# Kernel tuning notes

Hardware: AMD Instinct MI355X
Metric: run time of the kernel (lower is better)

## Reference

```python
import jax, jax.numpy as jnp
import numpy as np

NU, NI, D, E = 100000, 50000, 128, 800000

FLOAT_NAMES = ["emb_user", "emb_item"]
for _l in (1, 2):
    FLOAT_NAMES += [f"l{_l}_ui_pW1", f"l{_l}_ui_pb1", f"l{_l}_ui_pW2", f"l{_l}_ui_pb2"]
    for _e in ("ui", "iu"):
        FLOAT_NAMES += [f"l{_l}_{_e}_Wn", f"l{_l}_{_e}_bn", f"l{_l}_{_e}_Ws", f"l{_l}_{_e}_bs"]
FLOAT_NAMES += ["head_W", "head_b"]


def setup_inputs() -> dict:
    key = jax.random.key(0)
    shapes = {"emb_user": (NU, D), "emb_item": (NI, D), "head_W": (1, D), "head_b": (1,)}
    for n in FLOAT_NAMES:
        if n not in shapes:
            shapes[n] = (D, D) if n.endswith(("W1", "W2", "Wn", "Ws")) else (D,)
    inp = {}
    for i, n in enumerate(FLOAT_NAMES):
        inp[n] = jax.random.normal(jax.random.fold_in(key, i), shapes[n], jnp.float32) * 0.05
    inp["ue_src"] = jax.random.randint(jax.random.fold_in(key, 100), (E,), 0, NU)
    inp["ue_dst"] = jax.random.randint(jax.random.fold_in(key, 101), (E,), 0, NI)
    inp["iu_src"] = jax.random.randint(jax.random.fold_in(key, 102), (E,), 0, NI)
    inp["iu_dst"] = jax.random.randint(jax.random.fold_in(key, 103), (E,), 0, NU)
    inp["num_user"] = NU
    inp["num_item"] = NI
    return inp


def _scatter_mean(src, idx, n):
    # sum per segment / clamped count  (matches torch scatter_add_ + clamp(min=1))
    s = jax.ops.segment_sum(src, idx, num_segments=n)
    c = jax.ops.segment_sum(jnp.ones((src.shape[0],), src.dtype), idx, num_segments=n)
    return s / jnp.maximum(c, 1.0)[:, None]


def _forward(p, ue_src, ue_dst, iu_src, iu_dst, nu, ni):
    # hidden_dim == EMBED_DIM -> no input_proj, just ReLU on embedding tables
    xu = jax.nn.relu(p["emb_user"])  # [NU, D]
    xi = jax.nn.relu(p["emb_item"])  # [NI, D]
    for l in (1, 2):
        # PRMPSAGEConv: user -> item (item=dst predicts user/src features, aggregate residuals)
        h = jax.nn.relu(xi @ p[f"l{l}_ui_pW1"].T + p[f"l{l}_ui_pb1"])
        pred = h @ p[f"l{l}_ui_pW2"].T + p[f"l{l}_ui_pb2"]           # [NI, D]
        resid = xu[ue_src] - pred[ue_dst]                              # [E, D]
        agg_i = _scatter_mean(resid, ue_dst, ni)                       # [NI, D]
        out_i = (agg_i @ p[f"l{l}_ui_Wn"].T + p[f"l{l}_ui_bn"]
                 + xi @ p[f"l{l}_ui_Ws"].T + p[f"l{l}_ui_bs"])
        # BipartiteSAGEConv: item -> user (mean-aggregate src feats)
        agg_u = _scatter_mean(xi[iu_src], iu_dst, nu)                  # [NU, D]
        out_u = (agg_u @ p[f"l{l}_iu_Wn"].T + p[f"l{l}_iu_bn"]
                 + xu @ p[f"l{l}_iu_Ws"].T + p[f"l{l}_iu_bs"])
        # dropout is identity in eval; ReLU after each layer per original forward
        xu, xi = jax.nn.relu(out_u), jax.nn.relu(out_i)
    return (xu @ p["head_W"].T + p["head_b"])[:, 0]  # squeeze(-1) -> [NU]


def reference(emb_user, emb_item,
              l1_ui_pW1, l1_ui_pb1, l1_ui_pW2, l1_ui_pb2,
              l1_ui_Wn, l1_ui_bn, l1_ui_Ws, l1_ui_bs,
              l1_iu_Wn, l1_iu_bn, l1_iu_Ws, l1_iu_bs,
              l2_ui_pW1, l2_ui_pb1, l2_ui_pW2, l2_ui_pb2,
              l2_ui_Wn, l2_ui_bn, l2_ui_Ws, l2_ui_bs,
              l2_iu_Wn, l2_iu_bn, l2_iu_Ws, l2_iu_bs,
              head_W, head_b,
              ue_src, ue_dst, iu_src, iu_dst, num_user, num_item):
    floats = (emb_user, emb_item,
              l1_ui_pW1, l1_ui_pb1, l1_ui_pW2, l1_ui_pb2,
              l1_ui_Wn, l1_ui_bn, l1_ui_Ws, l1_ui_bs,
              l1_iu_Wn, l1_iu_bn, l1_iu_Ws, l1_iu_bs,
              l2_ui_pW1, l2_ui_pb1, l2_ui_pW2, l2_ui_pb2,
              l2_ui_Wn, l2_ui_bn, l2_ui_Ws, l2_ui_bs,
              l2_iu_Wn, l2_iu_bn, l2_iu_Ws, l2_iu_bs,
              head_W, head_b)
    p = dict(zip(FLOAT_NAMES, floats))
    return _forward(p, ue_src, ue_dst, iu_src, iu_dst, num_user, num_item)
```

## Files before the change

kernel.cpp:

```cpp
#include <hip/hip_runtime.h>
#include <hip/hip_bf16.h>

#define DD 128
#define PAD_I 64
#define PAD_U 48

typedef __attribute__((ext_vector_type(8))) short bf16x8;
typedef __attribute__((ext_vector_type(4))) float f32x4;

__device__ __forceinline__ unsigned short rne_bf16(float x) {
    unsigned int u = __float_as_uint(x);
    return (unsigned short)((u + 0x7FFFu + ((u >> 16) & 1u)) >> 16);
}

template <bool R>
__device__ __forceinline__ void load_split8(const float* __restrict__ p,
                                            bf16x8& hf, bf16x8& lf) {
    float4 v0 = *reinterpret_cast<const float4*>(p);
    float4 v1 = *reinterpret_cast<const float4*>(p + 4);
    float x[8] = {v0.x, v0.y, v0.z, v0.w, v1.x, v1.y, v1.z, v1.w};
#pragma unroll
    for (int j = 0; j < 8; j += 2) {
        float a = R ? fmaxf(x[j], 0.f) : x[j];
        float b = R ? fmaxf(x[j + 1], 0.f) : x[j + 1];
        __hip_bfloat162 h2 = __float22bfloat162_rn(make_float2(a, b));
        float2 hr = __bfloat1622float2(h2);
        __hip_bfloat162 l2 = __float22bfloat162_rn(make_float2(a - hr.x, b - hr.y));
        hf[j]     = (short)__bfloat16_as_ushort(h2.x);
        hf[j + 1] = (short)__bfloat16_as_ushort(h2.y);
        lf[j]     = (short)__bfloat16_as_ushort(l2.x);
        lf[j + 1] = (short)__bfloat16_as_ushort(l2.y);
    }
}


__global__ __launch_bounds__(256) void zeroi_k(int* __restrict__ p, int n) {
    int gid = blockIdx.x * 256 + threadIdx.x;
    if (gid < n) p[gid] = 0;
}

__global__ __launch_bounds__(256) void fill_k(const int* __restrict__ src,
                                              const int* __restrict__ dst,
                                              int* __restrict__ cur,
                                              int* __restrict__ pad, int PAD, int E) {
    int e = blockIdx.x * 256 + threadIdx.x;
    if (e >= E) return;
    int d = dst[e];
    int slot = atomicAdd(&cur[d], 1);
    if (slot < PAD) pad[(size_t)d * PAD + slot] = src[e];
}

template <bool RELU>
__device__ __forceinline__ void gather_body(const float* __restrict__ feat,
                                            const int* __restrict__ cur,
                                            const int* __restrict__ pad, int PAD,
                                            float* __restrict__ out, int N, int blk) {
    int row = blk * 4 + (threadIdx.x >> 6);
    if (row >= N) return;
    int lane = threadIdx.x & 63;
    int p = lane >> 4, c = lane & 15;
    int deg = cur[row]; if (deg > PAD) deg = PAD;
    const int* pl = pad + (size_t)row * PAD;

    float4 a0 = make_float4(0.f, 0.f, 0.f, 0.f);
    float4 a1 = make_float4(0.f, 0.f, 0.f, 0.f);
    float4 b0 = make_float4(0.f, 0.f, 0.f, 0.f);
    float4 b1 = make_float4(0.f, 0.f, 0.f, 0.f);
    int j = p;
    for (; j + 4 < deg; j += 8) {
        int s0 = pl[j];
        int s1 = pl[j + 4];
        const float* q0 = feat + (size_t)s0 * DD + c * 8;
        const float* q1 = feat + (size_t)s1 * DD + c * 8;
        float4 u0 = *reinterpret_cast<const float4*>(q0);
        float4 u1 = *reinterpret_cast<const float4*>(q0 + 4);
        float4 u2 = *reinterpret_cast<const float4*>(q1);
        float4 u3 = *reinterpret_cast<const float4*>(q1 + 4);
        if (RELU) {
            u0.x = fmaxf(u0.x, 0.f); u0.y = fmaxf(u0.y, 0.f); u0.z = fmaxf(u0.z, 0.f); u0.w = fmaxf(u0.w, 0.f);
            u1.x = fmaxf(u1.x, 0.f); u1.y = fmaxf(u1.y, 0.f); u1.z = fmaxf(u1.z, 0.f); u1.w = fmaxf(u1.w, 0.f);
            u2.x = fmaxf(u2.x, 0.f); u2.y = fmaxf(u2.y, 0.f); u2.z = fmaxf(u2.z, 0.f); u2.w = fmaxf(u2.w, 0.f);
            u3.x = fmaxf(u3.x, 0.f); u3.y = fmaxf(u3.y, 0.f); u3.z = fmaxf(u3.z, 0.f); u3.w = fmaxf(u3.w, 0.f);
        }
        a0.x += u0.x; a0.y += u0.y; a0.z += u0.z; a0.w += u0.w;
        a1.x += u1.x; a1.y += u1.y; a1.z += u1.z; a1.w += u1.w;
        b0.x += u2.x; b0.y += u2.y; b0.z += u2.z; b0.w += u2.w;
        b1.x += u3.x; b1.y += u3.y; b1.z += u3.z; b1.w += u3.w;
    }
    if (j < deg) {
        int s = pl[j];
        const float* q = feat + (size_t)s * DD + c * 8;
        float4 u0 = *reinterpret_cast<const float4*>(q);
        float4 u1 = *reinterpret_cast<const float4*>(q + 4);
        if (RELU) {
            u0.x = fmaxf(u0.x, 0.f); u0.y = fmaxf(u0.y, 0.f); u0.z = fmaxf(u0.z, 0.f); u0.w = fmaxf(u0.w, 0.f);
            u1.x = fmaxf(u1.x, 0.f); u1.y = fmaxf(u1.y, 0.f); u1.z = fmaxf(u1.z, 0.f); u1.w = fmaxf(u1.w, 0.f);
        }
        a0.x += u0.x; a0.y += u0.y; a0.z += u0.z; a0.w += u0.w;
        a1.x += u1.x; a1.y += u1.y; a1.z += u1.z; a1.w += u1.w;
    }
    a0.x += b0.x; a0.y += b0.y; a0.z += b0.z; a0.w += b0.w;
    a1.x += b1.x; a1.y += b1.y; a1.z += b1.z; a1.w += b1.w;

#pragma unroll
    for (int off = 16; off <= 32; off <<= 1) {
        a0.x += __shfl_xor(a0.x, off); a0.y += __shfl_xor(a0.y, off);
        a0.z += __shfl_xor(a0.z, off); a0.w += __shfl_xor(a0.w, off);
        a1.x += __shfl_xor(a1.x, off); a1.y += __shfl_xor(a1.y, off);
        a1.z += __shfl_xor(a1.z, off); a1.w += __shfl_xor(a1.w, off);
    }
    if (p == 0) {
        float iv = 1.0f / (float)(deg > 1 ? deg : 1);
        a0.x *= iv; a0.y *= iv; a0.z *= iv; a0.w *= iv;
        a1.x *= iv; a1.y *= iv; a1.z *= iv; a1.w *= iv;
        float* o = out + (size_t)row * DD + c * 8;
        *reinterpret_cast<float4*>(o) = a0;
        *reinterpret_cast<float4*>(o + 4) = a1;
    }
}

template <bool RELU>
__global__ __launch_bounds__(256) void gather_mean_k(const float* __restrict__ feat,
                                                     const int* __restrict__ cur,
                                                     const int* __restrict__ pad, int PAD,
                                                     float* __restrict__ out, int N) {
    gather_body<RELU>(feat, cur, pad, PAD, out, N, blockIdx.x);
}

template <bool RELU1, bool RELU2>
__global__ __launch_bounds__(256) void gather2_k(
        const float* __restrict__ feat1, const int* __restrict__ cur1,
        const int* __restrict__ pad1, int PAD1, float* __restrict__ out1, int N1, int nb1,
        const float* __restrict__ feat2, const int* __restrict__ cur2,
        const int* __restrict__ pad2, int PAD2, float* __restrict__ out2, int N2, int nb2) {
    int b = blockIdx.x;
    int which, idx;
    if (nb2 == 2 * nb1) {
        int tri = b / 3, rem = b - tri * 3;
        if (rem == 0) { which = 0; idx = tri; }
        else          { which = 1; idx = 2 * tri + rem - 1; }
    } else {
        which = (b < nb1) ? 0 : 1;
        idx = which ? (b - nb1) : b;
    }
    if (which == 0) gather_body<RELU1>(feat1, cur1, pad1, PAD1, out1, N1, idx);
    else            gather_body<RELU2>(feat2, cur2, pad2, PAD2, out2, N2, idx);
}

__global__ __launch_bounds__(256) void head_k(const float* __restrict__ x,
                                              const float* __restrict__ hw,
                                              const float* __restrict__ hb,
                                              float* __restrict__ out, int N) {
    int wid = threadIdx.x >> 6, lane = threadIdx.x & 63;
    int row = blockIdx.x * 4 + wid;
    if (row >= N) return;
    const float* xr = x + (size_t)row * DD;
    float v = xr[lane] * hw[lane] + xr[lane + 64] * hw[lane + 64];
    for (int off = 32; off > 0; off >>= 1) v += __shfl_down(v, off);
    if (lane == 0) out[row] = v + hb[0];
}


struct W12 { const float* p[12]; };

__global__ __launch_bounds__(256) void wsplit_k(W12 ws, unsigned short* __restrict__ hi,
                                                unsigned short* __restrict__ lo) {
    int idx = blockIdx.x * 256 + threadIdx.x;
    if (idx >= 12 * DD * DD) return;
    int m = idx >> 14, pk = idx & 16383;
    int j = pk & 7, lane = (pk >> 3) & 63, t = (pk >> 9) & 7, kc = (pk >> 12) & 3;
    int src = (t * 16 + (lane & 15)) * DD + kc * 32 + (lane >> 4) * 8 + j;
    float x = ws.p[m][src];
    unsigned short h = rne_bf16(x);
    float r = x - __uint_as_float((unsigned int)h << 16);
    hi[idx] = h;
    lo[idx] = rne_bf16(r);
}


template <bool RELX>
__global__ __launch_bounds__(256) void fused23_k(
        const float* __restrict__ X,
        const unsigned short* __restrict__ W1h, const unsigned short* __restrict__ W1l,
        const float* __restrict__ B1,
        const unsigned short* __restrict__ W2h, const unsigned short* __restrict__ W2l,
        const float* __restrict__ B2,
        float* __restrict__ Io, int N, const int* __restrict__ deg) {
    __shared__ __align__(16) float hl[64][DD + 4];

    const int tid = threadIdx.x;
    const int w = tid >> 6, l = tid & 63;
    const int l15 = l & 15, lq = l >> 4;

    const int rowA = blockIdx.x * 64 + w * 16 + l15;
    const int rA = rowA < N ? rowA : N - 1;
    const float* xp = X + (size_t)rA * DD;

    bf16x8 ah[4], al[4];
#pragma unroll
    for (int kc = 0; kc < 4; ++kc)
        load_split8<RELX>(xp + kc * 32 + lq * 8, ah[kc], al[kc]);

    f32x4 acc[8];
#pragma unroll
    for (int t = 0; t < 8; ++t) acc[t] = (f32x4){0.f, 0.f, 0.f, 0.f};

#pragma unroll
    for (int kc = 0; kc < 4; ++kc) {
        const size_t fb = ((size_t)(kc * 8) * 64 + l) * 8;
        bf16x8 bh[8], bl[8];
#pragma unroll
        for (int t = 0; t < 8; ++t) bh[t] = *reinterpret_cast<const bf16x8*>(W1h + fb + t * 512);
#pragma unroll
        for (int t = 0; t < 8; ++t) bl[t] = *reinterpret_cast<const bf16x8*>(W1l + fb + t * 512);
#pragma unroll
        for (int t = 0; t < 8; ++t)
            acc[t] = __builtin_amdgcn_mfma_f32_16x16x32_bf16(ah[kc], bh[t], acc[t], 0, 0, 0);
#pragma unroll
        for (int t = 0; t < 8; ++t)
            acc[t] = __builtin_amdgcn_mfma_f32_16x16x32_bf16(al[kc], bh[t], acc[t], 0, 0, 0);
#pragma unroll
        for (int t = 0; t < 8; ++t)
            acc[t] = __builtin_amdgcn_mfma_f32_16x16x32_bf16(ah[kc], bl[t], acc[t], 0, 0, 0);
    }

    const int lr0 = w * 16 + lq * 4;
#pragma unroll
    for (int t = 0; t < 8; ++t) {
        const int col = t * 16 + l15;
        const float b = B1[col];
#pragma unroll
        for (int r = 0; r < 4; ++r)
            hl[lr0 + r][col] = fmaxf(acc[t][r] + b, 0.f);
    }
    __syncthreads();

    bf16x8 ah2[4], al2[4];
#pragma unroll
    for (int kc = 0; kc < 4; ++kc)
        load_split8<false>(&hl[w * 16 + l15][kc * 32 + lq * 8], ah2[kc], al2[kc]);

#pragma unroll
    for (int t = 0; t < 8; ++t) acc[t] = (f32x4){0.f, 0.f, 0.f, 0.f};

#pragma unroll
    for (int kc = 0; kc < 4; ++kc) {
        const size_t fb = ((size_t)(kc * 8) * 64 + l) * 8;
        bf16x8 bh[8], bl[8];
#pragma unroll
        for (int t = 0; t < 8; ++t) bh[t] = *reinterpret_cast<const bf16x8*>(W2h + fb + t * 512);
#pragma unroll
        for (int t = 0; t < 8; ++t) bl[t] = *reinterpret_cast<const bf16x8*>(W2l + fb + t * 512);
#pragma unroll
        for (int t = 0; t < 8; ++t)
            acc[t] = __builtin_amdgcn_mfma_f32_16x16x32_bf16(ah2[kc], bh[t], acc[t], 0, 0, 0);
#pragma unroll
        for (int t = 0; t < 8; ++t)
            acc[t] = __builtin_amdgcn_mfma_f32_16x16x32_bf16(al2[kc], bh[t], acc[t], 0, 0, 0);
#pragma unroll
        for (int t = 0; t < 8; ++t)
            acc[t] = __builtin_amdgcn_mfma_f32_16x16x32_bf16(ah2[kc], bl[t], acc[t], 0, 0, 0);
    }

    const int orow0 = blockIdx.x * 64 + w * 16 + lq * 4;
#pragma unroll
    for (int t = 0; t < 8; ++t) {
        const int col = t * 16 + l15;
        const float b2v = B2[col];
#pragma unroll
        for (int r = 0; r < 4; ++r) {
            const int grow = orow0 + r;
            if (grow >= N) continue;
            float fl = deg[grow] > 0 ? 1.f : 0.f;
            float* op = Io + (size_t)grow * DD + col;
            *op = *op - (acc[t][r] + b2v) * fl;
        }
    }
}

template <bool RELX2>
__global__ __launch_bounds__(256) void gemm_dual_k(
        const float* __restrict__ X1,
        const unsigned short* __restrict__ W1h, const unsigned short* __restrict__ W1l,
        const float* __restrict__ B1,
        const float* __restrict__ X2,
        const unsigned short* __restrict__ W2h, const unsigned short* __restrict__ W2l,
        const float* __restrict__ B2,
        float* __restrict__ out, int N) {
    const int tid = threadIdx.x;
    const int w = tid >> 6, l = tid & 63;
    const int l15 = l & 15, lq = l >> 4;

    const int rowA = blockIdx.x * 64 + w * 16 + l15;
    const int rA = rowA < N ? rowA : N - 1;

    f32x4 acc[8];
#pragma unroll
    for (int t = 0; t < 8; ++t) acc[t] = (f32x4){0.f, 0.f, 0.f, 0.f};

    {
        bf16x8 ah[4], al[4];
#pragma unroll
        for (int kc = 0; kc < 4; ++kc)
            load_split8<false>(X1 + (size_t)rA * DD + kc * 32 + lq * 8, ah[kc], al[kc]);
#pragma unroll
        for (int kc = 0; kc < 4; ++kc) {
            const size_t fb = ((size_t)(kc * 8) * 64 + l) * 8;
            bf16x8 bh[8], bl[8];
#pragma unroll
            for (int t = 0; t < 8; ++t) bh[t] = *reinterpret_cast<const bf16x8*>(W1h + fb + t * 512);
#pragma unroll
            for (int t = 0; t < 8; ++t) bl[t] = *reinterpret_cast<const bf16x8*>(W1l + fb + t * 512);
#pragma unroll
            for (int t = 0; t < 8; ++t)
                acc[t] = __builtin_amdgcn_mfma_f32_16x16x32_bf16(ah[kc], bh[t], acc[t], 0, 0, 0);
#pragma unroll
            for (int t = 0; t < 8; ++t)
                acc[t] = __builtin_amdgcn_mfma_f32_16x16x32_bf16(al[kc], bh[t], acc[t], 0, 0, 0);
#pragma unroll
            for (int t = 0; t < 8; ++t)
                acc[t] = __builtin_amdgcn_mfma_f32_16x16x32_bf16(ah[kc], bl[t], acc[t], 0, 0, 0);
        }
    }
    {
        bf16x8 ah[4], al[4];
#pragma unroll
        for (int kc = 0; kc < 4; ++kc)
            load_split8<RELX2>(X2 + (size_t)rA * DD + kc * 32 + lq * 8, ah[kc], al[kc]);
#pragma unroll
        for (int kc = 0; kc < 4; ++kc) {
            const size_t fb = ((size_t)(kc * 8) * 64 + l) * 8;
            bf16x8 bh[8], bl[8];
#pragma unroll
            for (int t = 0; t < 8; ++t) bh[t] = *reinterpret_cast<const bf16x8*>(W2h + fb + t * 512);
#pragma unroll
            for (int t = 0; t < 8; ++t) bl[t] = *reinterpret_cast<const bf16x8*>(W2l + fb + t * 512);
#pragma unroll
            for (int t = 0; t < 8; ++t)
                acc[t] = __builtin_amdgcn_mfma_f32_16x16x32_bf16(ah[kc], bh[t], acc[t], 0, 0, 0);
#pragma unroll
            for (int t = 0; t < 8; ++t)
                acc[t] = __builtin_amdgcn_mfma_f32_16x16x32_bf16(al[kc], bh[t], acc[t], 0, 0, 0);
#pragma unroll
            for (int t = 0; t < 8; ++t)
                acc[t] = __builtin_amdgcn_mfma_f32_16x16x32_bf16(ah[kc], bl[t], acc[t], 0, 0, 0);
        }
    }

    const int orow0 = blockIdx.x * 64 + w * 16 + lq * 4;
#pragma unroll
    for (int t = 0; t < 8; ++t) {
        const int col = t * 16 + l15;
        const float bias = B1[col] + B2[col];
#pragma unroll
        for (int r = 0; r < 4; ++r) {
            const int grow = orow0 + r;
            if (grow >= N) continue;
            out[(size_t)grow * DD + col] = fmaxf(acc[t][r] + bias, 0.f);
        }
    }
}


extern "C" void kernel_launch(void* const* d_in, const int* in_sizes, int n_in,
                              void* d_out, int out_size, void* d_ws, size_t ws_size,
                              hipStream_t stream) {
    const float* emb_user = (const float*)d_in[0];
    const float* emb_item = (const float*)d_in[1];
    const float* head_W   = (const float*)d_in[26];
    const float* head_b   = (const float*)d_in[27];
    const int*   ue_src   = (const int*)d_in[28];
    const int*   ue_dst   = (const int*)d_in[29];
    const int*   iu_src   = (const int*)d_in[30];
    const int*   iu_dst   = (const int*)d_in[31];

    const int NU = in_sizes[0] / DD;
    const int NI = in_sizes[1] / DD;
    const int E  = in_sizes[28];

    const float* L[2][12];
    for (int l = 0; l < 2; ++l)
        for (int j = 0; j < 12; ++j) L[l][j] = (const float*)d_in[2 + l * 12 + j];

    const size_t SU = (size_t)NU * DD, SI = (size_t)NI * DD;
    const size_t WPLANE = 12 * (size_t)DD * DD;
    size_t need = 0;
    auto pad256 = [](size_t b) { return (b + 255) & ~(size_t)255; };
    need += 2 * pad256(SU * 4) + pad256(SI * 4);
    need += pad256((size_t)NI * 4) + pad256((size_t)NU * 4);
    need += pad256((size_t)NI * PAD_I * 4) + pad256((size_t)NU * PAD_U * 4);
    need += 2 * pad256(WPLANE * 2);
    if (ws_size < need) return;

    char* w = (char*)d_ws;
    auto alloc = [&](size_t bytes) { void* p = w; w += pad256(bytes); return p; };
    float* Ua    = (float*)alloc(SU * 4);
    float* Ub    = (float*)alloc(SU * 4);
    float* Ia    = (float*)alloc(SI * 4);
    int*   deg_i = (int*)alloc((size_t)NI * 4);
    int*   deg_u = (int*)alloc((size_t)NU * 4);
    int*   adj_i = (int*)alloc((size_t)NI * PAD_I * 4);
    int*   adj_u = (int*)alloc((size_t)NU * PAD_U * 4);
    unsigned short* Whi = (unsigned short*)alloc(WPLANE * 2);
    unsigned short* Wlo = (unsigned short*)alloc(WPLANE * 2);

    auto cdiv = [](long long a, long long b) { return (int)((a + b - 1) / b); };

    W12 ws;
    for (int l = 0; l < 2; ++l) {
        ws.p[l * 6 + 0] = L[l][0];
        ws.p[l * 6 + 1] = L[l][2];
        ws.p[l * 6 + 2] = L[l][4];
        ws.p[l * 6 + 3] = L[l][6];
        ws.p[l * 6 + 4] = L[l][8];
        ws.p[l * 6 + 5] = L[l][10];
    }
    wsplit_k<<<cdiv(WPLANE, 256), 256, 0, stream>>>(ws, Whi, Wlo);

    zeroi_k<<<cdiv(NI, 256), 256, 0, stream>>>(deg_i, NI);
    zeroi_k<<<cdiv(NU, 256), 256, 0, stream>>>(deg_u, NU);
    fill_k<<<cdiv(E, 256), 256, 0, stream>>>(ue_src, ue_dst, deg_i, adj_i, PAD_I, E);
    fill_k<<<cdiv(E, 256), 256, 0, stream>>>(iu_src, iu_dst, deg_u, adj_u, PAD_U, E);

    const int gI = cdiv(NI, 64), gU = cdiv(NU, 64);
    const int nbI = cdiv(NI, 4), nbU = cdiv(NU, 4);
    const size_t WM = (size_t)DD * DD;
    auto WH = [&](int l, int m) { return Whi + ((size_t)l * 6 + m) * WM; };
    auto WL = [&](int l, int m) { return Wlo + ((size_t)l * 6 + m) * WM; };

    gather2_k<true, true><<<nbI + nbU, 256, 0, stream>>>(
        emb_user, deg_i, adj_i, PAD_I, Ia, NI, nbI,
        emb_item, deg_u, adj_u, PAD_U, Ua, NU, nbU);
    gemm_dual_k<true><<<gU, 256, 0, stream>>>(Ua, WH(0,4), WL(0,4), L[0][9],
                                              emb_user, WH(0,5), WL(0,5), L[0][11], Ua, NU);
    fused23_k<true><<<gI, 256, 0, stream>>>(emb_item, WH(0,0), WL(0,0), L[0][1],
                                            WH(0,1), WL(0,1), L[0][3], Ia, NI, deg_i);
    gemm_dual_k<true><<<gI, 256, 0, stream>>>(Ia, WH(0,2), WL(0,2), L[0][5],
                                              emb_item, WH(0,3), WL(0,3), L[0][7], Ia, NI);

    gather_mean_k<false><<<nbU, 256, 0, stream>>>(Ia, deg_u, adj_u, PAD_U, Ub, NU);
    gemm_dual_k<false><<<gU, 256, 0, stream>>>(Ub, WH(1,4), WL(1,4), L[1][9],
                                               Ua, WH(1,5), WL(1,5), L[1][11], Ub, NU);

    head_k<<<cdiv(NU, 4), 256, 0, stream>>>(Ub, head_W, head_b, (float*)d_out, NU);
}
```

Before: 453.8 us.

## Co-schedule layer-1 user GEMM with layer-2 user gather in one launch

The layer-1 user-side dual GEMM is moved after the item-side kernels and merged with the layer-2 user gather into a single heterogeneous kernel. Block indices are interleaved so that roughly one GEMM block runs for every S gather blocks. The goal is to overlap MFMA-bound GEMM work with memory-bound gather work and to save one launch. In exchange there is more complex block-to-work mapping, and mixed block types may load-balance unevenly.

```diff
diff --git a/kernel.cpp b/kernel.cpp
--- a/kernel.cpp
+++ b/kernel.cpp
@@ -119,14 +119,6 @@
     }
 }
 
-template <bool RELU>
-__global__ __launch_bounds__(256) void gather_mean_k(const float* __restrict__ feat,
-                                                     const int* __restrict__ cur,
-                                                     const int* __restrict__ pad, int PAD,
-                                                     float* __restrict__ out, int N) {
-    gather_body<RELU>(feat, cur, pad, PAD, out, N, blockIdx.x);
-}
-
 template <bool RELU1, bool RELU2>
 __global__ __launch_bounds__(256) void gather2_k(
         const float* __restrict__ feat1, const int* __restrict__ cur1,
@@ -178,6 +170,123 @@
 }
 
 
+template <bool RELX2>
+__device__ __forceinline__ void gemm_dual_body(
+        const float* __restrict__ X1,
+        const unsigned short* __restrict__ W1h, const unsigned short* __restrict__ W1l,
+        const float* __restrict__ B1,
+        const float* __restrict__ X2,
+        const unsigned short* __restrict__ W2h, const unsigned short* __restrict__ W2l,
+        const float* __restrict__ B2,
+        float* __restrict__ out, int N, int blk) {
+    const int tid = threadIdx.x;
+    const int w = tid >> 6, l = tid & 63;
+    const int l15 = l & 15, lq = l >> 4;
+
+    const int rowA = blk * 64 + w * 16 + l15;
+    const int rA = rowA < N ? rowA : N - 1;
+
+    f32x4 acc[8];
+#pragma unroll
+    for (int t = 0; t < 8; ++t) acc[t] = (f32x4){0.f, 0.f, 0.f, 0.f};
+
+    {
+        bf16x8 ah[4], al[4];
+#pragma unroll
+        for (int kc = 0; kc < 4; ++kc)
+            load_split8<false>(X1 + (size_t)rA * DD + kc * 32 + lq * 8, ah[kc], al[kc]);
+#pragma unroll
+        for (int kc = 0; kc < 4; ++kc) {
+            const size_t fb = ((size_t)(kc * 8) * 64 + l) * 8;
+            bf16x8 bh[8], bl[8];
+#pragma unroll
+            for (int t = 0; t < 8; ++t) bh[t] = *reinterpret_cast<const bf16x8*>(W1h + fb + t * 512);
+#pragma unroll
+            for (int t = 0; t < 8; ++t) bl[t] = *reinterpret_cast<const bf16x8*>(W1l + fb + t * 512);
+#pragma unroll
+            for (int t = 0; t < 8; ++t)
+                acc[t] = __builtin_amdgcn_mfma_f32_16x16x32_bf16(ah[kc], bh[t], acc[t], 0, 0, 0);
+#pragma unroll
+            for (int t = 0; t < 8; ++t)
+                acc[t] = __builtin_amdgcn_mfma_f32_16x16x32_bf16(al[kc], bh[t], acc[t], 0, 0, 0);
+#pragma unroll
+            for (int t = 0; t < 8; ++t)
+                acc[t] = __builtin_amdgcn_mfma_f32_16x16x32_bf16(ah[kc], bl[t], acc[t], 0, 0, 0);
+        }
+    }
+    {
+        bf16x8 ah[4], al[4];
+#pragma unroll
+        for (int kc = 0; kc < 4; ++kc)
+            load_split8<RELX2>(X2 + (size_t)rA * DD + kc * 32 + lq * 8, ah[kc], al[kc]);
+#pragma unroll
+        for (int kc = 0; kc < 4; ++kc) {
+            const size_t fb = ((size_t)(kc * 8) * 64 + l) * 8;
+            bf16x8 bh[8], bl[8];
+#pragma unroll
+            for (int t = 0; t < 8; ++t) bh[t] = *reinterpret_cast<const bf16x8*>(W2h + fb + t * 512);
+#pragma unroll
+            for (int t = 0; t < 8; ++t) bl[t] = *reinterpret_cast<const bf16x8*>(W2l + fb + t * 512);
+#pragma unroll
+            for (int t = 0; t < 8; ++t)
+                acc[t] = __builtin_amdgcn_mfma_f32_16x16x32_bf16(ah[kc], bh[t], acc[t], 0, 0, 0);
+#pragma unroll
+            for (int t = 0; t < 8; ++t)
+                acc[t] = __builtin_amdgcn_mfma_f32_16x16x32_bf16(al[kc], bh[t], acc[t], 0, 0, 0);
+#pragma unroll
+            for (int t = 0; t < 8; ++t)
+                acc[t] = __builtin_amdgcn_mfma_f32_16x16x32_bf16(ah[kc], bl[t], acc[t], 0, 0, 0);
+        }
+    }
+
+    const int orow0 = blk * 64 + w * 16 + lq * 4;
+#pragma unroll
+    for (int t = 0; t < 8; ++t) {
+        const int col = t * 16 + l15;
+        const float bias = B1[col] + B2[col];
+#pragma unroll
+        for (int r = 0; r < 4; ++r) {
+            const int grow = orow0 + r;
+            if (grow >= N) continue;
+            out[(size_t)grow * DD + col] = fmaxf(acc[t][r] + bias, 0.f);
+        }
+    }
+}
+
+template <bool RELX2>
+__global__ __launch_bounds__(256) void gemm_dual_k(
+        const float* __restrict__ X1,
+        const unsigned short* __restrict__ W1h, const unsigned short* __restrict__ W1l,
+        const float* __restrict__ B1,
+        const float* __restrict__ X2,
+        const unsigned short* __restrict__ W2h, const unsigned short* __restrict__ W2l,
+        const float* __restrict__ B2,
+        float* __restrict__ out, int N) {
+    gemm_dual_body<RELX2>(X1, W1h, W1l, B1, X2, W2h, W2l, B2, out, N, blockIdx.x);
+}
+
+template <bool RELX2, bool RELUF>
+__global__ __launch_bounds__(256) void gemm_gather_k(
+        const float* __restrict__ X1,
+        const unsigned short* __restrict__ W1h, const unsigned short* __restrict__ W1l,
+        const float* __restrict__ B1,
+        const float* __restrict__ X2,
+        const unsigned short* __restrict__ W2h, const unsigned short* __restrict__ W2l,
+        const float* __restrict__ B2,
+        float* __restrict__ out, int N, int nG, int S,
+        const float* __restrict__ feat, const int* __restrict__ cur,
+        const int* __restrict__ pad, int PAD, float* __restrict__ gout, int GN) {
+    int b = blockIdx.x;
+    int g = b / S, r = b - g * S;
+    if (r == 0 && g < nG) {
+        gemm_dual_body<RELX2>(X1, W1h, W1l, B1, X2, W2h, W2l, B2, out, N, g);
+    } else {
+        int gemsBefore = g + (r > 0 ? 1 : 0);
+        if (gemsBefore > nG) gemsBefore = nG;
+        gather_body<RELUF>(feat, cur, pad, PAD, gout, GN, b - gemsBefore);
+    }
+}
+
 template <bool RELX>
 __global__ __launch_bounds__(256) void fused23_k(
         const float* __restrict__ X,
@@ -274,89 +383,6 @@
             float fl = deg[grow] > 0 ? 1.f : 0.f;
             float* op = Io + (size_t)grow * DD + col;
             *op = *op - (acc[t][r] + b2v) * fl;
-        }
-    }
-}
-
-template <bool RELX2>
-__global__ __launch_bounds__(256) void gemm_dual_k(
-        const float* __restrict__ X1,
-        const unsigned short* __restrict__ W1h, const unsigned short* __restrict__ W1l,
-        const float* __restrict__ B1,
-        const float* __restrict__ X2,
-        const unsigned short* __restrict__ W2h, const unsigned short* __restrict__ W2l,
-        const float* __restrict__ B2,
-        float* __restrict__ out, int N) {
-    const int tid = threadIdx.x;
-    const int w = tid >> 6, l = tid & 63;
-    const int l15 = l & 15, lq = l >> 4;
-
-    const int rowA = blockIdx.x * 64 + w * 16 + l15;
-    const int rA = rowA < N ? rowA : N - 1;
-
-    f32x4 acc[8];
-#pragma unroll
-    for (int t = 0; t < 8; ++t) acc[t] = (f32x4){0.f, 0.f, 0.f, 0.f};
-
-    {
-        bf16x8 ah[4], al[4];
-#pragma unroll
-        for (int kc = 0; kc < 4; ++kc)
-            load_split8<false>(X1 + (size_t)rA * DD + kc * 32 + lq * 8, ah[kc], al[kc]);
-#pragma unroll
-        for (int kc = 0; kc < 4; ++kc) {
-            const size_t fb = ((size_t)(kc * 8) * 64 + l) * 8;
-            bf16x8 bh[8], bl[8];
-#pragma unroll
-            for (int t = 0; t < 8; ++t) bh[t] = *reinterpret_cast<const bf16x8*>(W1h + fb + t * 512);
-#pragma unroll
-            for (int t = 0; t < 8; ++t) bl[t] = *reinterpret_cast<const bf16x8*>(W1l + fb + t * 512);
-#pragma unroll
-            for (int t = 0; t < 8; ++t)
-                acc[t] = __builtin_amdgcn_mfma_f32_16x16x32_bf16(ah[kc], bh[t], acc[t], 0, 0, 0);
-#pragma unroll
-            for (int t = 0; t < 8; ++t)
-                acc[t] = __builtin_amdgcn_mfma_f32_16x16x32_bf16(al[kc], bh[t], acc[t], 0, 0, 0);
-#pragma unroll
-            for (int t = 0; t < 8; ++t)
-                acc[t] = __builtin_amdgcn_mfma_f32_16x16x32_bf16(ah[kc], bl[t], acc[t], 0, 0, 0);
-        }
-    }
-    {
-        bf16x8 ah[4], al[4];
-#pragma unroll
-        for (int kc = 0; kc < 4; ++kc)
-            load_split8<RELX2>(X2 + (size_t)rA * DD + kc * 32 + lq * 8, ah[kc], al[kc]);
-#pragma unroll
-        for (int kc = 0; kc < 4; ++kc) {
-            const size_t fb = ((size_t)(kc * 8) * 64 + l) * 8;
-            bf16x8 bh[8], bl[8];
-#pragma unroll
-            for (int t = 0; t < 8; ++t) bh[t] = *reinterpret_cast<const bf16x8*>(W2h + fb + t * 512);
-#pragma unroll
-            for (int t = 0; t < 8; ++t) bl[t] = *reinterpret_cast<const bf16x8*>(W2l + fb + t * 512);
-#pragma unroll
-            for (int t = 0; t < 8; ++t)
-                acc[t] = __builtin_amdgcn_mfma_f32_16x16x32_bf16(ah[kc], bh[t], acc[t], 0, 0, 0);
-#pragma unroll
-            for (int t = 0; t < 8; ++t)
-                acc[t] = __builtin_amdgcn_mfma_f32_16x16x32_bf16(al[kc], bh[t], acc[t], 0, 0, 0);
-#pragma unroll
-            for (int t = 0; t < 8; ++t)
-                acc[t] = __builtin_amdgcn_mfma_f32_16x16x32_bf16(ah[kc], bl[t], acc[t], 0, 0, 0);
-        }
-    }
-
-    const int orow0 = blockIdx.x * 64 + w * 16 + lq * 4;
-#pragma unroll
-    for (int t = 0; t < 8; ++t) {
-        const int col = t * 16 + l15;
-        const float bias = B1[col] + B2[col];
-#pragma unroll
-        for (int r = 0; r < 4; ++r) {
-            const int grow = orow0 + r;
-            if (grow >= N) continue;
-            out[(size_t)grow * DD + col] = fmaxf(acc[t][r] + bias, 0.f);
         }
     }
 }
@@ -431,14 +457,20 @@
     gather2_k<true, true><<<nbI + nbU, 256, 0, stream>>>(
         emb_user, deg_i, adj_i, PAD_I, Ia, NI, nbI,
         emb_item, deg_u, adj_u, PAD_U, Ua, NU, nbU);
-    gemm_dual_k<true><<<gU, 256, 0, stream>>>(Ua, WH(0,4), WL(0,4), L[0][9],
-                                              emb_user, WH(0,5), WL(0,5), L[0][11], Ua, NU);
     fused23_k<true><<<gI, 256, 0, stream>>>(emb_item, WH(0,0), WL(0,0), L[0][1],
                                             WH(0,1), WL(0,1), L[0][3], Ia, NI, deg_i);
     gemm_dual_k<true><<<gI, 256, 0, stream>>>(Ia, WH(0,2), WL(0,2), L[0][5],
                                               emb_item, WH(0,3), WL(0,3), L[0][7], Ia, NI);
 
-    gather_mean_k<false><<<nbU, 256, 0, stream>>>(Ia, deg_u, adj_u, PAD_U, Ub, NU);
+    {
+        int total = gU + nbU;
+        int S = total / gU;
+        gemm_gather_k<true, false><<<total, 256, 0, stream>>>(
+            Ua, WH(0,4), WL(0,4), L[0][9],
+            emb_user, WH(0,5), WL(0,5), L[0][11], Ua, NU, gU, S,
+            Ia, deg_u, adj_u, PAD_U, Ub, NU);
+    }
+
     gemm_dual_k<false><<<gU, 256, 0, stream>>>(Ub, WH(1,4), WL(1,4), L[1][9],
                                                Ua, WH(1,5), WL(1,5), L[1][11], Ub, NU);
 
```

Result: slower. 934.7 us (+106.0%).
